# Kernel tuning notes

Measured on AMD Instinct MI355X. Metric: run time of the kernel, lower is better.

## Reference

```python
import jax, jax.numpy as jnp
import numpy as np

B, NQ, L, E, K = 64, 1024, 128, 8192, 2
LN_EPS = 1e-5


def setup_inputs() -> dict:
    key = jax.random.key(0)
    ks = jax.random.split(key, 16)
    s1 = 1.0 / np.sqrt(2 * L + 1)
    s2 = 1.0 / np.sqrt(L)
    s3 = 1.0 / np.sqrt(2 * L)
    return {
        "z0": jax.random.normal(ks[0], (B, L), jnp.float32),
        "edge_index": jax.random.randint(ks[1], (2, E), 0, NQ, jnp.int64),
        "edge_attr": jax.random.normal(ks[2], (E,), jnp.float32),
        "n_qubits": NQ,
        # edge MLP params, stacked over K message-passing rounds
        "e_w1": jax.random.normal(ks[3], (K, L, 2 * L + 1), jnp.float32) * s1,
        "e_b1": jnp.zeros((K, L), jnp.float32),
        "e_w2": jax.random.normal(ks[4], (K, L, L), jnp.float32) * s2,
        "e_b2": jnp.zeros((K, L), jnp.float32),
        # node MLP params
        "n_w1": jax.random.normal(ks[5], (K, L, 2 * L), jnp.float32) * s3,
        "n_b1": jnp.zeros((K, L), jnp.float32),
        "ln_g": jnp.ones((K, L), jnp.float32),
        "ln_b": jnp.zeros((K, L), jnp.float32),
        "n_w2": jax.random.normal(ks[6], (K, L, L), jnp.float32) * s2,
        "n_b2": jnp.zeros((K, L), jnp.float32),
    }


def reference(z0, edge_index, edge_attr, n_qubits,
              e_w1, e_b1, e_w2, e_b2,
              n_w1, n_b1, ln_g, ln_b, n_w2, n_b2):
    b, l = z0.shape
    src, tgt = edge_index[0], edge_index[1]
    e_ = src.shape[0]
    # broadcast latent z0 to every node: h [B, N, L]
    h = jnp.broadcast_to(z0[:, None, :], (b, n_qubits, l))
    e = jnp.broadcast_to(edge_attr[None, :, None], (b, e_, 1))  # [B, E, 1]
    k_rounds = e_w1.shape[0]
    for k in range(k_rounds):
        hi = h[:, src, :]  # gather source node feats [B, E, L]
        hj = h[:, tgt, :]  # gather target node feats [B, E, L]
        inp_e = jnp.concatenate([hi, hj, e], axis=-1)  # [B, E, 2L+1]
        m = jax.nn.relu(inp_e @ e_w1[k].T + e_b1[k]) @ e_w2[k].T + e_b2[k]
        # scatter_add messages back to source nodes
        m_agg = jnp.zeros_like(h).at[:, src, :].add(m)
        inp_n = jnp.concatenate([h, m_agg], axis=-1)  # [B, N, 2L]
        x = jax.nn.relu(inp_n @ n_w1[k].T + n_b1[k])
        mu = x.mean(axis=-1, keepdims=True)
        var = ((x - mu) ** 2).mean(axis=-1, keepdims=True)
        x = (x - mu) * jax.lax.rsqrt(var + LN_EPS) * ln_g[k] + ln_b[k]
        # Dropout(p=0.1) is identity in eval mode
        h = x @ n_w2[k].T + n_b2[k] + h  # residual
    return h.mean(axis=1)  # [B, L]
```

## Files before the change

### kernel.cpp

```cpp
#include <hip/hip_runtime.h>

#define B_   64
#define NQ_  1024
#define L_   128
#define E_   8192
#define M_   (B_*NQ_)
#define LDP  136
#define TILE 2176

typedef unsigned short u16;
typedef unsigned int   u32;
typedef unsigned long long u64;
typedef __attribute__((ext_vector_type(8))) short short8;
typedef __attribute__((ext_vector_type(4))) float floatx4;

#define WVB() __builtin_amdgcn_wave_barrier()

__device__ __forceinline__ int imax2(int a, int b) { return a > b ? a : b; }
__device__ __forceinline__ int imin2(int a, int b) { return a < b ? a : b; }

__device__ __forceinline__ u16 f2bf(float f) {
    union { float f; u32 u; } v; v.f = f;
    return (u16)((v.u + 0x7fffu + ((v.u >> 16) & 1u)) >> 16);
}
__device__ __forceinline__ float bf2f(u16 u) {
    union { u32 u; float f; } v; v.u = ((u32)u) << 16;
    return v.f;
}
__device__ __forceinline__ float bf2f_lo(u32 jv) { return __uint_as_float(jv << 16); }
__device__ __forceinline__ float bf2f_hi(u32 jv) { return __uint_as_float(jv & 0xffff0000u); }
__device__ __forceinline__ floatx4 mfma16(short8 a, short8 b, floatx4 c) {
    return __builtin_amdgcn_mfma_f32_16x16x32_bf16(a, b, c, 0, 0, 0);
}
__device__ __forceinline__ short8 sfrag(const u16* t, int r0, int kb, int lane) {
    return *(const short8*)(t + (r0 + (lane & 15)) * LDP + kb * 32 + (lane >> 4) * 8);
}
__device__ __forceinline__ short8 wfrag(const u16* wf, int nt, int kb, int lane) {
    return *(const short8*)(wf + (((kb << 3) + nt) * 64 + lane) * 8);
}
__device__ __forceinline__ void frag_flush(const u16* t, u16* wf, int nt, int lane) {
#pragma unroll
    for (int kb = 0; kb < 4; ++kb)
        *(short8*)(wf + (((kb << 3) + nt) * 64 + lane) * 8) = sfrag(t, 0, kb, lane);
}
__device__ __forceinline__ short8 frag_cvt(const float* base, int r0, int ld, int kb, int lane) {
    const float* p = base + (size_t)(r0 + (lane & 15)) * ld + kb * 32 + (lane >> 4) * 8;
    short8 s;
#pragma unroll
    for (int j = 0; j < 8; ++j) s[j] = (short)f2bf(p[j]);
    return s;
}
__device__ __forceinline__ void tile_store(u16* t, const floatx4* acc, int lane) {
    int col = lane & 15, qd = lane >> 4;
#pragma unroll
    for (int nt = 0; nt < 8; ++nt)
#pragma unroll
        for (int r = 0; r < 4; ++r)
            t[(qd * 4 + r) * LDP + nt * 16 + col] = f2bf(acc[nt][r]);
}
__device__ __forceinline__ void tile_flush(const u16* t, u16* g, int lane) {
#pragma unroll
    for (int it = 0; it < 4; ++it) {
        int chunk = it * 64 + lane, row = chunk >> 4, c8 = chunk & 15;
        *(uint4*)(g + (size_t)row * 128 + c8 * 8) = *(const uint4*)(t + row * LDP + c8 * 8);
    }
}
__device__ __forceinline__ int blk_swz() {
    int r = blockIdx.x;
    int b = (((r >> 3) & 7) << 3) | (r & 7);
    return b * 16 + (r >> 6);
}

struct P {
    const int* ei; const float* attr; const float* z0;
    const float* e_w1; const float* e_b1; const float* e_w2; const float* e_b2;
    const float* n_w1; const float* n_b1; const float* ln_g; const float* ln_b;
    const float* n_w2; const float* n_b2;
    int* ofs; int2* ta; int* perm; float* degf;
    u16* wf;
    u16* w_n20;
    float* wl; float* vb2;
    float* rx; float* rci; float* rcj; float* rh; float* mx0;
    u16* c0t; u16* t1g; u16* ci1; u16* cj1;
    float* out;
};

__global__ __launch_bounds__(256) void k_setup(P p) {
    __shared__ __align__(16) char smem[17408];
    int tid = threadIdx.x, blk = blockIdx.x;
    int lane = tid & 63, w = tid >> 6, col = lane & 15, qd = lane >> 4;

    if (blk == 0) {
        __shared__ int cnt[1024];
        __shared__ int wsum[4];
        __shared__ int dh[64];
        __shared__ int db[64];
        __shared__ int flag;
#pragma unroll
        for (int i = 0; i < 4; ++i) cnt[tid + i * 256] = 0;
        if (tid < 64) dh[tid] = 0;
        if (tid == 0) flag = 1;
        __syncthreads();
        if (tid < 100 && p.ei[2 * tid + 1] != 0) atomicAnd(&flag, 0);
        __syncthreads();
        int i64 = flag;
        for (int e = tid; e < E_; e += 256) {
            int s = i64 ? p.ei[2 * e] : p.ei[e];
            atomicAdd(&cnt[s], 1);
        }
        __syncthreads();
        int q0 = tid * 4;
        int c0 = cnt[q0], c1 = cnt[q0 + 1], c2 = cnt[q0 + 2], c3 = cnt[q0 + 3];
        int tsum = c0 + c1 + c2 + c3, incl = tsum;
#pragma unroll
        for (int o = 1; o < 64; o <<= 1) {
            int t = __shfl_up(incl, o, 64);
            if (lane >= o) incl += t;
        }
        if (lane == 63) wsum[w] = incl;
        atomicAdd(&dh[imin2(c0, 63)], 1); atomicAdd(&dh[imin2(c1, 63)], 1);
        atomicAdd(&dh[imin2(c2, 63)], 1); atomicAdd(&dh[imin2(c3, 63)], 1);
        __syncthreads();
        int wo = 0;
        for (int i = 0; i < w; ++i) wo += wsum[i];
        int base = wo + incl - tsum;
        p.ofs[q0] = base; p.ofs[q0 + 1] = base + c0;
        p.ofs[q0 + 2] = base + c0 + c1; p.ofs[q0 + 3] = base + c0 + c1 + c2;
        p.degf[q0] = (float)c0; p.degf[q0 + 1] = (float)c1;
        p.degf[q0 + 2] = (float)c2; p.degf[q0 + 3] = (float)c3;
        if (tid == 0) p.ofs[NQ_] = E_;
        __syncthreads();
        cnt[q0] = base; cnt[q0 + 1] = base + c0;
        cnt[q0 + 2] = base + c0 + c1; cnt[q0 + 3] = base + c0 + c1 + c2;
        if (tid < 64) {
            int v = dh[tid], inc = v;
#pragma unroll
            for (int o = 1; o < 64; o <<= 1) {
                int t = __shfl_up(inc, o, 64);
                if (tid >= o) inc += t;
            }
            db[tid] = inc - v;
        }
        __syncthreads();
        for (int e = tid; e < E_; e += 256) {
            int s = i64 ? p.ei[2 * e]        : p.ei[e];
            int t = i64 ? p.ei[2 * (E_ + e)] : p.ei[E_ + e];
            int pos = atomicAdd(&cnt[s], 1);
            p.ta[pos] = make_int2(t << 6, __float_as_int(p.attr[e]));
        }
        p.perm[atomicAdd(&db[imin2(c0, 63)], 1)] = q0;
        p.perm[atomicAdd(&db[imin2(c1, 63)], 1)] = q0 + 1;
        p.perm[atomicAdd(&db[imin2(c2, 63)], 1)] = q0 + 2;
        p.perm[atomicAdd(&db[imin2(c3, 63)], 1)] = q0 + 3;
        if (tid == 0) p.ta[E_] = make_int2(0, 0);
    } else if (blk <= 2) {
        int base = (blk - 1) * 8192;
        for (int idx = tid; idx < 8192; idx += 256)
            p.w_n20[base + idx] = f2bf(p.n_w2[base + idx]);
    } else if (blk == 3) {
        const float* src = p.n_w2 + 16384;
        u16* dst = p.wf + 5 * 16384;
        for (int pr = w; pr < 32; pr += 4) {
            int kb = pr >> 3, nt = pr & 7;
            const float* s = src + (nt * 16 + col) * 128 + kb * 32 + qd * 8;
            short8 v;
#pragma unroll
            for (int j = 0; j < 8; ++j) v[j] = (short)f2bf(s[j]);
            *(short8*)(dst + (pr * 64 + lane) * 8) = v;
        }
    } else if (blk <= 13) {
        int g = (blk - 4) >> 1, part = (blk - 4) & 1;
        const float* Pm; const float* Q; int ldp; u16* D;
        switch (g) {
            case 0:  Pm = p.n_w1 + 128;             ldp = 256; Q = p.e_w2;         D = p.wf;             break;
            case 1:  Pm = p.n_w1 + 32768 + 128;     ldp = 256; Q = p.e_w2 + 16384; D = p.wf + 4 * 16384; break;
            case 2:  Pm = p.e_w1 + 128 * 257;       ldp = 257; Q = p.n_w2;         D = p.wf + 1 * 16384; break;
            case 3:  Pm = p.e_w1 + 128 * 257 + 128; ldp = 257; Q = p.n_w2;         D = p.wf + 2 * 16384; break;
            default: Pm = p.n_w1 + 32768;           ldp = 256; Q = p.n_w2;         D = p.wf + 3 * 16384; break;
        }
        int tile = part * 4 + w;
        int r0 = tile * 16;
        floatx4 acc[8] = {};
#pragma unroll
        for (int kb = 0; kb < 4; ++kb) {
            short8 a = frag_cvt(Pm, r0, ldp, kb, lane);
#pragma unroll
            for (int nt = 0; nt < 8; ++nt) {
                short8 bq;
#pragma unroll
                for (int j = 0; j < 8; ++j)
                    bq[j] = (short)f2bf(Q[(kb * 32 + qd * 8 + j) * 128 + nt * 16 + col]);
                acc[nt] = mfma16(a, bq, acc[nt]);
            }
        }
        u16* slot = (u16*)smem + w * TILE;
        tile_store(slot, acc, lane); WVB();
        frag_flush(slot, D, tile, lane);
    } else if (blk == 14) {
        int r0 = w * 16;
        floatx4 acc[8] = {};
#pragma unroll
        for (int kb = 0; kb < 4; ++kb) {
            short8 a = frag_cvt(p.z0, r0, 128, kb, lane);
#pragma unroll
            for (int nt = 0; nt < 8; ++nt)
                acc[nt] = mfma16(a, frag_cvt(p.n_w1, nt * 16, 256, kb, lane), acc[nt]);
        }
#pragma unroll
        for (int nt = 0; nt < 8; ++nt) {
            int cg = nt * 16 + col; float bv = p.n_b1[cg];
#pragma unroll
            for (int r = 0; r < 4; ++r) p.rx[(r0 + qd * 4 + r) * 128 + cg] = acc[nt][r] + bv;
        }
    } else if (blk <= 17) {
        int r0 = w * 16;
        const float* Wp; int ld; const float* bias; float* dst;
        if (blk == 15)      { Wp = p.e_w1 + 128 * 257;       ld = 257; bias = p.e_b1 + 128; dst = p.rci; }
        else if (blk == 16) { Wp = p.e_w1 + 128 * 257 + 128; ld = 257; bias = nullptr;      dst = p.rcj; }
        else                { Wp = p.n_w1 + 32768;           ld = 256; bias = p.n_b1 + 128; dst = p.rh;  }
        floatx4 acc[8] = {};
#pragma unroll
        for (int kb = 0; kb < 4; ++kb) {
            short8 a;
            int rr = (r0 + col) * 128, kk = kb * 32 + qd * 8;
#pragma unroll
            for (int j = 0; j < 8; ++j) a[j] = (short)f2bf(p.z0[rr + kk + j] + p.n_b2[kk + j]);
#pragma unroll
            for (int nt = 0; nt < 8; ++nt)
                acc[nt] = mfma16(a, frag_cvt(Wp, nt * 16, ld, kb, lane), acc[nt]);
        }
#pragma unroll
        for (int nt = 0; nt < 8; ++nt) {
            int cg = nt * 16 + col;
            float bv = bias ? bias[cg] : 0.0f;
#pragma unroll
            for (int r = 0; r < 4; ++r) dst[(r0 + qd * 4 + r) * 128 + cg] = acc[nt][r] + bv;
        }
    } else if (blk == 18) {
        int r0 = w * 16;
        floatx4 a1[8] = {};
#pragma unroll
        for (int kb = 0; kb < 4; ++kb) {
            short8 a = frag_cvt(p.z0, r0, 128, kb, lane);
#pragma unroll
            for (int nt = 0; nt < 8; ++nt) {
                a1[nt] = mfma16(a, frag_cvt(p.e_w1,       nt * 16, 257, kb, lane), a1[nt]);
                a1[nt] = mfma16(a, frag_cvt(p.e_w1 + 128, nt * 16, 257, kb, lane), a1[nt]);
            }
        }
#pragma unroll
        for (int nt = 0; nt < 8; ++nt) {
            float bv = p.e_b1[nt * 16 + col];
#pragma unroll
            for (int r = 0; r < 4; ++r) a1[nt][r] += bv;
        }
        u16* slot = (u16*)smem + w * TILE;
        tile_store(slot, a1, lane); WVB();
        tile_flush(slot, p.c0t + (size_t)r0 * 128, lane);
    } else {
        int k = tid >> 7, c = tid & 127;
        const float4* wp = (const float4*)(p.n_w1 + k * 32768 + c * 256 + 128);
        const float4* bp = (const float4*)(p.e_b2 + k * 128);
        float s0 = 0.f, s1 = 0.f, s2 = 0.f, s3 = 0.f;
#pragma unroll
        for (int n4 = 0; n4 < 32; ++n4) {
            float4 a = wp[n4], bv = bp[n4];
            s0 += a.x * bv.x; s1 += a.y * bv.y; s2 += a.z * bv.z; s3 += a.w * bv.w;
        }
        p.vb2[tid] = (s0 + s1) + (s2 + s3);
        p.wl[tid]  = p.e_w1[k * 128 * 257 + c * 257 + 256];
        for (int i = tid; i < 8192; i += 256) p.mx0[i] = 0.0f;
    }
}

__device__ __forceinline__ void load_qmap(int* qmap, const int* perm,
                                          int blk, int w, int lane) {
    int W = (blk & 15) * 4 + w;
    int g0 = W, g1 = 127 - W;
    if (lane < 16)
        qmap[w * 16 + lane] = perm[lane < 8 ? g0 * 8 + lane : g1 * 8 + lane - 8];
    WVB();
}

__global__ __launch_bounds__(256, 4) void k_node0(P p) {
    __shared__ __align__(16) char smem[35072];
    u16* xt = (u16*)smem;
    u16* ob = (u16*)(smem + 17408);
    int* qmap = (int*)(smem + 34816);
    int tid = threadIdx.x, lane = tid & 63, w = tid >> 6;
    int col = lane & 15, qd = lane >> 4;
    int blk = blk_swz();
    int rowbase = blk * 64 + w * 16;
    int b = blk >> 4;
    load_qmap(qmap, p.perm, blk, w, lane);

    {
        u32 cv = ((const u32*)p.c0t)[b * 64 + lane];
        float cx = bf2f((u16)(cv & 0xffffu)), cy = bf2f((u16)(cv >> 16));
        float2 wl2 = ((const float2*)p.wl)[lane];
        const int* tay = (const int*)p.ta;
        for (int g2 = 0; g2 < 2; ++g2) {
            int st[8], en[8];
            float ax[8] = {}, ay[8] = {};
#pragma unroll
            for (int j = 0; j < 8; ++j) {
                int q = qmap[w * 16 + g2 * 8 + j];
                st[j] = p.ofs[q]; en[j] = p.ofs[q + 1];
            }
            int mn = en[0] - st[0], mx = mn;
#pragma unroll
            for (int j = 1; j < 8; ++j) {
                mn = imin2(mn, en[j] - st[j]); mx = imax2(mx, en[j] - st[j]);
            }
            float ac[8];
#pragma unroll
            for (int j = 0; j < 8; ++j) {
                int last = en[j] - 1;
                int safe = st[j] < en[j] ? st[j] : (last >= 0 ? last : 0);
                ac[j] = __int_as_float(tay[2 * safe + 1]);
            }
            for (int k2 = 0; k2 < mn; ++k2) {
                float an[8];
#pragma unroll
                for (int j = 0; j < 8; ++j) an[j] = __int_as_float(tay[2 * (st[j] + k2 + 1) + 1]);
#pragma unroll
                for (int j = 0; j < 8; ++j) {
                    ax[j] += fmaxf(cx + ac[j] * wl2.x, 0.f);
                    ay[j] += fmaxf(cy + ac[j] * wl2.y, 0.f);
                    ac[j] = an[j];
                }
            }
            for (int k2 = mn; k2 < mx; ++k2) {
                float an[8];
#pragma unroll
                for (int j = 0; j < 8; ++j) {
                    int idx = st[j] + k2 + 1, last = en[j] - 1;
                    int safe = idx < en[j] ? idx : (last >= 0 ? last : 0);
                    an[j] = __int_as_float(tay[2 * safe + 1]);
                }
#pragma unroll
                for (int j = 0; j < 8; ++j) {
                    bool v = st[j] + k2 < en[j];
                    ax[j] += v ? fmaxf(cx + ac[j] * wl2.x, 0.f) : 0.f;
                    ay[j] += v ? fmaxf(cy + ac[j] * wl2.y, 0.f) : 0.f;
                    ac[j] = an[j];
                }
            }
#pragma unroll
            for (int j = 0; j < 8; ++j) {
                int r = g2 * 8 + j;
                u32* tp = (u32*)(xt + (size_t)w * TILE + r * LDP);
                tp[lane] = (u32)f2bf(ax[j]) | ((u32)f2bf(ay[j]) << 16);
            }
        }
    }
    WVB();

    floatx4 xa[8] = {};
#pragma unroll
    for (int kb = 0; kb < 4; ++kb) {
        short8 a = sfrag(xt + w * TILE, 0, kb, lane);
#pragma unroll
        for (int nt = 0; nt < 8; ++nt) xa[nt] = mfma16(a, wfrag(p.wf, nt, kb, lane), xa[nt]);
    }
    WVB();
    float s8[8] = {};
#pragma unroll
    for (int nt = 0; nt < 8; ++nt) {
        int cg = nt * 16 + col;
        float base = p.rx[b * 128 + cg], vb = p.vb2[cg];
#pragma unroll
        for (int r = 0; r < 4; ++r) {
            int q = qmap[w * 16 + qd * 4 + r];
            xa[nt][r] = fmaxf(xa[nt][r] + base + p.degf[q] * vb, 0.f);
        }
    }
#pragma unroll
    for (int r = 0; r < 4; ++r) {
        float s = 0.f, s2 = 0.f;
#pragma unroll
        for (int nt = 0; nt < 8; ++nt) { float v = xa[nt][r]; s += v; s2 += v * v; }
#pragma unroll
        for (int o = 1; o < 16; o <<= 1) { s += __shfl_xor(s, o, 64); s2 += __shfl_xor(s2, o, 64); }
        float mu = s * (1.f / 128.f), var = s2 * (1.f / 128.f) - mu * mu;
        float rs = rsqrtf(var + 1e-5f);
#pragma unroll
        for (int nt = 0; nt < 8; ++nt) {
            int cg = nt * 16 + col;
            float xv = (xa[nt][r] - mu) * rs * p.ln_g[cg] + p.ln_b[cg];
            xa[nt][r] = xv;
            s8[nt] += xv;
        }
    }
    tile_store(xt + w * TILE, xa, lane);
#pragma unroll
    for (int nt = 0; nt < 8; ++nt) {
        s8[nt] += __shfl_xor(s8[nt], 16, 64);
        s8[nt] += __shfl_xor(s8[nt], 32, 64);
    }
    if (lane < 16) {
#pragma unroll
        for (int nt = 0; nt < 8; ++nt)
            atomicAdd(p.mx0 + b * 128 + nt * 16 + lane, s8[nt]);
    }
    WVB();
#pragma unroll
    for (int ph = 0; ph < 3; ++ph) {
        const u16* wfp = p.wf + ((ph == 0) ? 1 : (ph == 1) ? 2 : 3) * 16384;
        const float* rt = (ph == 0) ? p.rci : (ph == 1) ? p.rcj : p.rh;
        floatx4 ca[8] = {};
#pragma unroll
        for (int kb = 0; kb < 4; ++kb) {
            short8 a = sfrag(xt + w * TILE, 0, kb, lane);
#pragma unroll
            for (int nt = 0; nt < 8; ++nt) ca[nt] = mfma16(a, wfrag(wfp, nt, kb, lane), ca[nt]);
        }
#pragma unroll
        for (int nt = 0; nt < 8; ++nt) {
            float rc = rt[b * 128 + nt * 16 + col];
#pragma unroll
            for (int r = 0; r < 4; ++r) ca[nt][r] += rc;
        }
        if (ph == 2) {
            u64* t1f = (u64*)p.t1g;
            int tile = blk * 4 + w;
#pragma unroll
            for (int nt = 0; nt < 8; ++nt) {
                u32 lo = (u32)f2bf(ca[nt][0]) | ((u32)f2bf(ca[nt][1]) << 16);
                u32 hi = (u32)f2bf(ca[nt][2]) | ((u32)f2bf(ca[nt][3]) << 16);
                t1f[(size_t)(tile * 8 + nt) * 64 + lane] = (u64)lo | ((u64)hi << 32);
            }
        } else if (ph == 0) {
            tile_store(ob + w * TILE, ca, lane);
            WVB();
            tile_flush(ob + w * TILE, p.ci1 + (size_t)rowbase * 128, lane);
            WVB();
        } else {
            tile_store(ob + w * TILE, ca, lane);
            WVB();
#pragma unroll
            for (int it = 0; it < 4; ++it) {
                int chunk = it * 64 + lane, row = chunk >> 4, c8 = chunk & 15;
                int q = qmap[w * 16 + row];
                *(uint4*)(p.cj1 + ((size_t)b * NQ_ + q) * 128 + c8 * 8) =
                    *(const uint4*)(ob + w * TILE + row * LDP + c8 * 8);
            }
            WVB();
        }
    }
}

__global__ __launch_bounds__(256, 4) void k_node1(P p) {
    __shared__ __align__(16) char smem[35072];
    u16* xt = (u16*)smem;
    u16* ob = (u16*)(smem + 17408);
    int* qmap = (int*)(smem + 34816);
    int tid = threadIdx.x, lane = tid & 63, w = tid >> 6;
    int col = lane & 15, qd = lane >> 4;
    int blk = blk_swz();
    int rowbase = blk * 64 + w * 16;
    int b = blk >> 4;
    load_qmap(qmap, p.perm, blk, w, lane);

    {
        float2 wl2 = ((const float2*)(p.wl + 128))[lane];
        const u32* cip = (const u32*)p.ci1;
        const u32* cjp = (const u32*)p.cj1 + (size_t)b * NQ_ * 64;
        for (int g2 = 0; g2 < 2; ++g2) {
            int st[8], en[8];
            float ax[8] = {}, ay[8] = {}, cx[8], cy[8];
#pragma unroll
            for (int j = 0; j < 8; ++j) {
                int prow = rowbase + g2 * 8 + j;
                u32 cv = cip[(size_t)prow * 64 + lane];
                cx[j] = bf2f((u16)(cv & 0xffffu)); cy[j] = bf2f((u16)(cv >> 16));
                int q = qmap[w * 16 + g2 * 8 + j];
                st[j] = p.ofs[q]; en[j] = p.ofs[q + 1];
            }
            int mn = en[0] - st[0], mx = mn;
#pragma unroll
            for (int j = 1; j < 8; ++j) {
                mn = imin2(mn, en[j] - st[j]); mx = imax2(mx, en[j] - st[j]);
            }
            int tc[8]; float ac[8];
#pragma unroll
            for (int j = 0; j < 8; ++j) {
                int last = en[j] - 1;
                int safe = st[j] < en[j] ? st[j] : (last >= 0 ? last : 0);
                int2 tv = p.ta[safe];
                tc[j] = tv.x; ac[j] = __int_as_float(tv.y);
            }
            for (int k2 = 0; k2 < mn; ++k2) {
                u32 jv[8];
#pragma unroll
                for (int j = 0; j < 8; ++j) jv[j] = cjp[(u32)(tc[j] + lane)];
                int2 tv[8];
#pragma unroll
                for (int j = 0; j < 8; ++j) tv[j] = p.ta[st[j] + k2 + 1];
#pragma unroll
                for (int j = 0; j < 8; ++j) {
                    ax[j] += fmaxf(cx[j] + bf2f_lo(jv[j]) + ac[j] * wl2.x, 0.f);
                    ay[j] += fmaxf(cy[j] + bf2f_hi(jv[j]) + ac[j] * wl2.y, 0.f);
                    tc[j] = tv[j].x; ac[j] = __int_as_float(tv[j].y);
                }
            }
            for (int k2 = mn; k2 < mx; ++k2) {
                u32 jv[8];
#pragma unroll
                for (int j = 0; j < 8; ++j) jv[j] = cjp[(u32)(tc[j] + lane)];
                int2 tv[8];
#pragma unroll
                for (int j = 0; j < 8; ++j) {
                    int idx = st[j] + k2 + 1, last = en[j] - 1;
                    int safe = idx < en[j] ? idx : (last >= 0 ? last : 0);
                    tv[j] = p.ta[safe];
                }
#pragma unroll
                for (int j = 0; j < 8; ++j) {
                    bool v = st[j] + k2 < en[j];
                    float vx = fmaxf(cx[j] + bf2f_lo(jv[j]) + ac[j] * wl2.x, 0.f);
                    float vy = fmaxf(cy[j] + bf2f_hi(jv[j]) + ac[j] * wl2.y, 0.f);
                    ax[j] += v ? vx : 0.f;
                    ay[j] += v ? vy : 0.f;
                    tc[j] = tv[j].x; ac[j] = __int_as_float(tv[j].y);
                }
            }
#pragma unroll
            for (int j = 0; j < 8; ++j) {
                int r = g2 * 8 + j;
                u32* tp = (u32*)(xt + (size_t)w * TILE + r * LDP);
                tp[lane] = (u32)f2bf(ax[j]) | ((u32)f2bf(ay[j]) << 16);
            }
        }
    }
    WVB();

    const u16* wc1 = p.wf + 4 * 16384;
    floatx4 xa[8] = {};
#pragma unroll
    for (int kb = 0; kb < 4; ++kb) {
        short8 a = sfrag(xt + w * TILE, 0, kb, lane);
#pragma unroll
        for (int nt = 0; nt < 8; ++nt) xa[nt] = mfma16(a, wfrag(wc1, nt, kb, lane), xa[nt]);
    }
    const float* vb21 = p.vb2 + 128;
    const u64* t1f = (const u64*)p.t1g;
    int tile = blk * 4 + w;
#pragma unroll
    for (int nt = 0; nt < 8; ++nt) {
        int cg = nt * 16 + col;
        float vb = vb21[cg];
        u64 tv = t1f[(size_t)(tile * 8 + nt) * 64 + lane];
        float tvf[4] = { bf2f((u16)tv),         bf2f((u16)(tv >> 16)),
                         bf2f((u16)(tv >> 32)), bf2f((u16)(tv >> 48)) };
#pragma unroll
        for (int r = 0; r < 4; ++r) {
            int q = qmap[w * 16 + qd * 4 + r];
            xa[nt][r] = fmaxf(xa[nt][r] + tvf[r] + p.degf[q] * vb, 0.f);
        }
    }
#pragma unroll
    for (int r = 0; r < 4; ++r) {
        float s = 0.f, s2 = 0.f;
#pragma unroll
        for (int nt = 0; nt < 8; ++nt) { float v = xa[nt][r]; s += v; s2 += v * v; }
#pragma unroll
        for (int o = 1; o < 16; o <<= 1) { s += __shfl_xor(s, o, 64); s2 += __shfl_xor(s2, o, 64); }
        float mu = s * (1.f / 128.f), var = s2 * (1.f / 128.f) - mu * mu;
        float rs = rsqrtf(var + 1e-5f);
#pragma unroll
        for (int nt = 0; nt < 8; ++nt) {
            int cg = nt * 16 + col;
            xa[nt][r] = (xa[nt][r] - mu) * rs * p.ln_g[128 + cg] + p.ln_b[128 + cg];
        }
    }
    const u16* n21 = p.wf + 5 * 16384;
    float s8[8] = {};
    tile_store(ob + w * TILE, xa, lane);
    WVB();
    {
        floatx4 ma[8] = {};
#pragma unroll
        for (int kb = 0; kb < 4; ++kb) {
            short8 a = sfrag(ob + w * TILE, 0, kb, lane);
#pragma unroll
            for (int nt = 0; nt < 8; ++nt) ma[nt] = mfma16(a, wfrag(n21, nt, kb, lane), ma[nt]);
        }
#pragma unroll
        for (int nt = 0; nt < 8; ++nt)
#pragma unroll
            for (int r = 0; r < 4; ++r) s8[nt] += ma[nt][r];
    }
#pragma unroll
    for (int nt = 0; nt < 8; ++nt) {
        s8[nt] += __shfl_xor(s8[nt], 16, 64);
        s8[nt] += __shfl_xor(s8[nt], 32, 64);
    }
    if (lane < 16) {
#pragma unroll
        for (int nt = 0; nt < 8; ++nt)
            atomicAdd(p.out + b * 128 + nt * 16 + lane, s8[nt] * (1.f / 1024.f));
    }
    if ((blk & 15) == 0 && tid < 128) {
        int c = tid;
        const float* mx = p.mx0 + b * 128;
        float s = 0.f;
#pragma unroll
        for (int k8 = 0; k8 < 16; ++k8) {
            short8 wv = *(const short8*)(p.w_n20 + c * 128 + k8 * 8);
            const float* mxp = mx + k8 * 8;
#pragma unroll
            for (int j = 0; j < 8; ++j) s += mxp[j] * bf2f((u16)wv[j]);
        }
        float acc = p.z0[b * 128 + c] + p.n_b2[c] + p.n_b2[128 + c] + s * (1.f / 1024.f);
        atomicAdd(p.out + b * 128 + c, acc);
    }
}

extern "C" void kernel_launch(void* const* d_in, const int* in_sizes, int n_in,
                              void* d_out, int out_size, void* d_ws, size_t ws_size,
                              hipStream_t stream) {
    P p;
    p.z0   = (const float*)d_in[0];
    p.ei   = (const int*)d_in[1];
    p.attr = (const float*)d_in[2];
    p.e_w1 = (const float*)d_in[4];
    p.e_b1 = (const float*)d_in[5];
    p.e_w2 = (const float*)d_in[6];
    p.e_b2 = (const float*)d_in[7];
    p.n_w1 = (const float*)d_in[8];
    p.n_b1 = (const float*)d_in[9];
    p.ln_g = (const float*)d_in[10];
    p.ln_b = (const float*)d_in[11];
    p.n_w2 = (const float*)d_in[12];
    p.n_b2 = (const float*)d_in[13];
    p.out  = (float*)d_out;

    const size_t H = (size_t)M_ * L_;
    float* f  = (float*)d_ws;
    p.degf = f;
    p.wl   = f + 1024;
    p.vb2  = p.wl + 256;
    p.rx   = p.vb2 + 256;
    p.rci  = p.rx + 8192;
    p.rcj  = p.rci + 8192;
    p.rh   = p.rcj + 8192;
    p.mx0  = p.rh + 8192;
    p.ofs  = (int*)(p.mx0 + 8192);
    p.perm = p.ofs + 1056;
    p.ta   = (int2*)(p.perm + 1024);
    p.wf    = (u16*)(p.ta + E_ + 8);
    p.w_n20 = p.wf + 6 * 16384;
    p.c0t   = p.w_n20 + 16384;
    p.t1g   = p.c0t + 8192;
    p.ci1   = p.t1g + H;
    p.cj1   = p.ci1 + H;

    hipMemsetAsync(p.out, 0, 8192 * sizeof(float), stream);

    k_setup<<<20, 256, 0, stream>>>(p);
    k_node0<<<1024, 256, 0, stream>>>(p);
    k_node1<<<1024, 256, 0, stream>>>(p);
}
```

Before: 192.0 us.

## Split node1 into 128-thread blocks of 16 rows and stage setup weights via LDS

k_node1 now launches 4096 blocks of two waves, each block covering one 16-row tile. Each wave gathers messages for 8 of those rows, with separate min/max trip counts per group of four rows to reduce divergent tail work. Both waves then compute the first node GEMM redundantly, and only wave 0 runs the second GEMM and the output atomics. The aim is higher occupancy and more parallelism to hide latency in the irregular edge gather, at the price of redundant MFMA work and extra block barriers. Separately, k_setup transposes the Q weight chunks through LDS so global reads are coalesced float4 loads instead of strided scalar loads.

```diff
diff --git a/kernel.cpp b/kernel.cpp
--- a/kernel.cpp
+++ b/kernel.cpp
@@ -86,24 +86,24 @@
 };
 
 __global__ __launch_bounds__(256) void k_setup(P p) {
-    __shared__ __align__(16) char smem[17408];
+    __shared__ __align__(16) char smem[35072];
     int tid = threadIdx.x, blk = blockIdx.x;
     int lane = tid & 63, w = tid >> 6, col = lane & 15, qd = lane >> 4;
 
     if (blk == 0) {
-        __shared__ int cnt[1024];
-        __shared__ int wsum[4];
-        __shared__ int dh[64];
-        __shared__ int db[64];
-        __shared__ int flag;
+        int* cnt  = (int*)smem;
+        int* wsum = cnt + 1024;
+        int* dh   = wsum + 4;
+        int* db   = dh + 64;
+        int* flag = db + 64;
 #pragma unroll
         for (int i = 0; i < 4; ++i) cnt[tid + i * 256] = 0;
         if (tid < 64) dh[tid] = 0;
-        if (tid == 0) flag = 1;
+        if (tid == 0) *flag = 1;
         __syncthreads();
-        if (tid < 100 && p.ei[2 * tid + 1] != 0) atomicAnd(&flag, 0);
+        if (tid < 100 && p.ei[2 * tid + 1] != 0) atomicAnd(flag, 0);
         __syncthreads();
-        int i64 = flag;
+        int i64 = *flag;
         for (int e = tid; e < E_; e += 256) {
             int s = i64 ? p.ei[2 * e] : p.ei[e];
             atomicAdd(&cnt[s], 1);
@@ -178,22 +178,34 @@
             case 3:  Pm = p.e_w1 + 128 * 257 + 128; ldp = 257; Q = p.n_w2;         D = p.wf + 2 * 16384; break;
             default: Pm = p.n_w1 + 32768;           ldp = 256; Q = p.n_w2;         D = p.wf + 3 * 16384; break;
         }
+        float* QT  = (float*)smem;
+        u16* slots = (u16*)(smem + 16896);
         int tile = part * 4 + w;
         int r0 = tile * 16;
         floatx4 acc[8] = {};
-#pragma unroll
         for (int kb = 0; kb < 4; ++kb) {
+            __syncthreads();
+#pragma unroll
+            for (int i = 0; i < 4; ++i) {
+                int off = (tid + i * 256) * 4;
+                int r = off >> 7, c = off & 127;
+                float4 v = *(const float4*)(Q + (size_t)(kb * 32 + r) * 128 + c);
+                QT[(c + 0) * 33 + r] = v.x; QT[(c + 1) * 33 + r] = v.y;
+                QT[(c + 2) * 33 + r] = v.z; QT[(c + 3) * 33 + r] = v.w;
+            }
+            __syncthreads();
             short8 a = frag_cvt(Pm, r0, ldp, kb, lane);
 #pragma unroll
             for (int nt = 0; nt < 8; ++nt) {
                 short8 bq;
 #pragma unroll
                 for (int j = 0; j < 8; ++j)
-                    bq[j] = (short)f2bf(Q[(kb * 32 + qd * 8 + j) * 128 + nt * 16 + col]);
+                    bq[j] = (short)f2bf(QT[(nt * 16 + col) * 33 + qd * 8 + j]);
                 acc[nt] = mfma16(a, bq, acc[nt]);
             }
         }
-        u16* slot = (u16*)smem + w * TILE;
+        __syncthreads();
+        u16* slot = slots + w * TILE;
         tile_store(slot, acc, lane); WVB();
         frag_flush(slot, D, tile, lane);
     } else if (blk == 14) {
@@ -271,15 +283,6 @@
         p.wl[tid]  = p.e_w1[k * 128 * 257 + c * 257 + 256];
         for (int i = tid; i < 8192; i += 256) p.mx0[i] = 0.0f;
     }
-}
-
-__device__ __forceinline__ void load_qmap(int* qmap, const int* perm,
-                                          int blk, int w, int lane) {
-    int W = (blk & 15) * 4 + w;
-    int g0 = W, g1 = 127 - W;
-    if (lane < 16)
-        qmap[w * 16 + lane] = perm[lane < 8 ? g0 * 8 + lane : g1 * 8 + lane - 8];
-    WVB();
 }
 
 __global__ __launch_bounds__(256, 4) void k_node0(P p) {
@@ -292,7 +295,12 @@
     int blk = blk_swz();
     int rowbase = blk * 64 + w * 16;
     int b = blk >> 4;
-    load_qmap(qmap, p.perm, blk, w, lane);
+    {
+        int W = (blk & 15) * 4 + w;
+        if (lane < 16)
+            qmap[w * 16 + lane] = p.perm[lane < 8 ? W * 8 + lane : (127 - W) * 8 + lane - 8];
+        WVB();
+    }
 
     {
         u32 cv = ((const u32*)p.c0t)[b * 64 + lane];
@@ -450,120 +458,158 @@
     }
 }
 
-__global__ __launch_bounds__(256, 4) void k_node1(P p) {
-    __shared__ __align__(16) char smem[35072];
+__global__ __launch_bounds__(128, 8) void k_node1(P p) {
+    __shared__ __align__(16) char smem[4480];
     u16* xt = (u16*)smem;
-    u16* ob = (u16*)(smem + 17408);
-    int* qmap = (int*)(smem + 34816);
+    int* qmap = (int*)(smem + 4352);
     int tid = threadIdx.x, lane = tid & 63, w = tid >> 6;
     int col = lane & 15, qd = lane >> 4;
-    int blk = blk_swz();
-    int rowbase = blk * 64 + w * 16;
-    int b = blk >> 4;
-    load_qmap(qmap, p.perm, blk, w, lane);
+    int r4 = blockIdx.x;
+    int b  = (((r4 >> 3) & 7) << 3) | (r4 & 7);
+    int nb = b * 64 + (r4 >> 6);
+    int W  = nb & 63;
+    if (tid < 16) qmap[tid] = p.perm[tid < 8 ? W * 8 + tid : (127 - W) * 8 + tid - 8];
+    __syncthreads();
 
     {
         float2 wl2 = ((const float2*)(p.wl + 128))[lane];
         const u32* cip = (const u32*)p.ci1;
         const u32* cjp = (const u32*)p.cj1 + (size_t)b * NQ_ * 64;
-        for (int g2 = 0; g2 < 2; ++g2) {
-            int st[8], en[8];
-            float ax[8] = {}, ay[8] = {}, cx[8], cy[8];
+        int rr[8], st[8], en[8];
+        float ax[8] = {}, ay[8] = {}, cx[8], cy[8];
+#pragma unroll
+        for (int j = 0; j < 8; ++j) {
+            rr[j] = w * 4 + (j & 3) + 8 * (j >> 2);
+            int prow = nb * 16 + rr[j];
+            u32 cv = cip[(size_t)prow * 64 + lane];
+            cx[j] = bf2f((u16)(cv & 0xffffu)); cy[j] = bf2f((u16)(cv >> 16));
+            int q = qmap[rr[j]];
+            st[j] = p.ofs[q]; en[j] = p.ofs[q + 1];
+        }
+        int mA = en[0] - st[0], MA = mA, mB = en[4] - st[4], MB = mB;
+#pragma unroll
+        for (int j = 1; j < 4; ++j) {
+            mA = imin2(mA, en[j] - st[j]); MA = imax2(MA, en[j] - st[j]);
+        }
+#pragma unroll
+        for (int j = 5; j < 8; ++j) {
+            mB = imin2(mB, en[j] - st[j]); MB = imax2(MB, en[j] - st[j]);
+        }
+        int m8 = imin2(mA, mB);
+        int tc[8]; float ac[8];
+#pragma unroll
+        for (int j = 0; j < 8; ++j) {
+            int last = en[j] - 1;
+            int safe = st[j] < en[j] ? st[j] : (last >= 0 ? last : 0);
+            int2 tv = p.ta[safe];
+            tc[j] = tv.x; ac[j] = __int_as_float(tv.y);
+        }
+        for (int k2 = 0; k2 < m8; ++k2) {
+            u32 jv[8];
+#pragma unroll
+            for (int j = 0; j < 8; ++j) jv[j] = cjp[(u32)(tc[j] + lane)];
+            int2 tv[8];
+#pragma unroll
+            for (int j = 0; j < 8; ++j) tv[j] = p.ta[st[j] + k2 + 1];
 #pragma unroll
             for (int j = 0; j < 8; ++j) {
-                int prow = rowbase + g2 * 8 + j;
-                u32 cv = cip[(size_t)prow * 64 + lane];
-                cx[j] = bf2f((u16)(cv & 0xffffu)); cy[j] = bf2f((u16)(cv >> 16));
-                int q = qmap[w * 16 + g2 * 8 + j];
-                st[j] = p.ofs[q]; en[j] = p.ofs[q + 1];
-            }
-            int mn = en[0] - st[0], mx = mn;
-#pragma unroll
-            for (int j = 1; j < 8; ++j) {
-                mn = imin2(mn, en[j] - st[j]); mx = imax2(mx, en[j] - st[j]);
-            }
-            int tc[8]; float ac[8];
-#pragma unroll
-            for (int j = 0; j < 8; ++j) {
-                int last = en[j] - 1;
-                int safe = st[j] < en[j] ? st[j] : (last >= 0 ? last : 0);
-                int2 tv = p.ta[safe];
-                tc[j] = tv.x; ac[j] = __int_as_float(tv.y);
-            }
-            for (int k2 = 0; k2 < mn; ++k2) {
-                u32 jv[8];
-#pragma unroll
-                for (int j = 0; j < 8; ++j) jv[j] = cjp[(u32)(tc[j] + lane)];
-                int2 tv[8];
-#pragma unroll
-                for (int j = 0; j < 8; ++j) tv[j] = p.ta[st[j] + k2 + 1];
-#pragma unroll
-                for (int j = 0; j < 8; ++j) {
-                    ax[j] += fmaxf(cx[j] + bf2f_lo(jv[j]) + ac[j] * wl2.x, 0.f);
-                    ay[j] += fmaxf(cy[j] + bf2f_hi(jv[j]) + ac[j] * wl2.y, 0.f);
-                    tc[j] = tv[j].x; ac[j] = __int_as_float(tv[j].y);
-                }
-            }
-            for (int k2 = mn; k2 < mx; ++k2) {
-                u32 jv[8];
-#pragma unroll
-                for (int j = 0; j < 8; ++j) jv[j] = cjp[(u32)(tc[j] + lane)];
-                int2 tv[8];
-#pragma unroll
-                for (int j = 0; j < 8; ++j) {
-                    int idx = st[j] + k2 + 1, last = en[j] - 1;
-                    int safe = idx < en[j] ? idx : (last >= 0 ? last : 0);
-                    tv[j] = p.ta[safe];
-                }
-#pragma unroll
-                for (int j = 0; j < 8; ++j) {
-                    bool v = st[j] + k2 < en[j];
-                    float vx = fmaxf(cx[j] + bf2f_lo(jv[j]) + ac[j] * wl2.x, 0.f);
-                    float vy = fmaxf(cy[j] + bf2f_hi(jv[j]) + ac[j] * wl2.y, 0.f);
-                    ax[j] += v ? vx : 0.f;
-                    ay[j] += v ? vy : 0.f;
-                    tc[j] = tv[j].x; ac[j] = __int_as_float(tv[j].y);
-                }
-            }
-#pragma unroll
-            for (int j = 0; j < 8; ++j) {
-                int r = g2 * 8 + j;
-                u32* tp = (u32*)(xt + (size_t)w * TILE + r * LDP);
-                tp[lane] = (u32)f2bf(ax[j]) | ((u32)f2bf(ay[j]) << 16);
-            }
-        }
-    }
-    WVB();
+                ax[j] += fmaxf(cx[j] + bf2f_lo(jv[j]) + ac[j] * wl2.x, 0.f);
+                ay[j] += fmaxf(cy[j] + bf2f_hi(jv[j]) + ac[j] * wl2.y, 0.f);
+                tc[j] = tv[j].x; ac[j] = __int_as_float(tv[j].y);
+            }
+        }
+        for (int k2 = m8; k2 < MA; ++k2) {
+            u32 jv[4];
+#pragma unroll
+            for (int j = 0; j < 4; ++j) jv[j] = cjp[(u32)(tc[j] + lane)];
+            int2 tv[4];
+#pragma unroll
+            for (int j = 0; j < 4; ++j) {
+                int idx = st[j] + k2 + 1, last = en[j] - 1;
+                int safe = idx < en[j] ? idx : (last >= 0 ? last : 0);
+                tv[j] = p.ta[safe];
+            }
+#pragma unroll
+            for (int j = 0; j < 4; ++j) {
+                bool v = st[j] + k2 < en[j];
+                float vx = fmaxf(cx[j] + bf2f_lo(jv[j]) + ac[j] * wl2.x, 0.f);
+                float vy = fmaxf(cy[j] + bf2f_hi(jv[j]) + ac[j] * wl2.y, 0.f);
+                ax[j] += v ? vx : 0.f;
+                ay[j] += v ? vy : 0.f;
+                tc[j] = tv[j].x; ac[j] = __int_as_float(tv[j].y);
+            }
+        }
+        for (int k2 = m8; k2 < mB; ++k2) {
+            u32 jv[4];
+#pragma unroll
+            for (int j = 4; j < 8; ++j) jv[j - 4] = cjp[(u32)(tc[j] + lane)];
+            int2 tv[4];
+#pragma unroll
+            for (int j = 4; j < 8; ++j) tv[j - 4] = p.ta[st[j] + k2 + 1];
+#pragma unroll
+            for (int j = 4; j < 8; ++j) {
+                ax[j] += fmaxf(cx[j] + bf2f_lo(jv[j - 4]) + ac[j] * wl2.x, 0.f);
+                ay[j] += fmaxf(cy[j] + bf2f_hi(jv[j - 4]) + ac[j] * wl2.y, 0.f);
+                tc[j] = tv[j - 4].x; ac[j] = __int_as_float(tv[j - 4].y);
+            }
+        }
+        for (int k2 = imax2(m8, mB); k2 < MB; ++k2) {
+            u32 jv[4];
+#pragma unroll
+            for (int j = 4; j < 8; ++j) jv[j - 4] = cjp[(u32)(tc[j] + lane)];
+            int2 tv[4];
+#pragma unroll
+            for (int j = 4; j < 8; ++j) {
+                int idx = st[j] + k2 + 1, last = en[j] - 1;
+                int safe = idx < en[j] ? idx : (last >= 0 ? last : 0);
+                tv[j - 4] = p.ta[safe];
+            }
+#pragma unroll
+            for (int j = 4; j < 8; ++j) {
+                bool v = st[j] + k2 < en[j];
+                float vx = fmaxf(cx[j] + bf2f_lo(jv[j - 4]) + ac[j] * wl2.x, 0.f);
+                float vy = fmaxf(cy[j] + bf2f_hi(jv[j - 4]) + ac[j] * wl2.y, 0.f);
+                ax[j] += v ? vx : 0.f;
+                ay[j] += v ? vy : 0.f;
+                tc[j] = tv[j - 4].x; ac[j] = __int_as_float(tv[j - 4].y);
+            }
+        }
+#pragma unroll
+        for (int j = 0; j < 8; ++j) {
+            u32* tp = (u32*)(xt + rr[j] * LDP);
+            tp[lane] = (u32)f2bf(ax[j]) | ((u32)f2bf(ay[j]) << 16);
+        }
+    }
+    __syncthreads();
 
     const u16* wc1 = p.wf + 4 * 16384;
-    floatx4 xa[8] = {};
+    floatx4 x1[8] = {};
 #pragma unroll
     for (int kb = 0; kb < 4; ++kb) {
-        short8 a = sfrag(xt + w * TILE, 0, kb, lane);
-#pragma unroll
-        for (int nt = 0; nt < 8; ++nt) xa[nt] = mfma16(a, wfrag(wc1, nt, kb, lane), xa[nt]);
+        short8 a = sfrag(xt, 0, kb, lane);
+#pragma unroll
+        for (int nt = 0; nt < 8; ++nt) x1[nt] = mfma16(a, wfrag(wc1, nt, kb, lane), x1[nt]);
     }
     const float* vb21 = p.vb2 + 128;
     const u64* t1f = (const u64*)p.t1g;
-    int tile = blk * 4 + w;
 #pragma unroll
     for (int nt = 0; nt < 8; ++nt) {
         int cg = nt * 16 + col;
         float vb = vb21[cg];
-        u64 tv = t1f[(size_t)(tile * 8 + nt) * 64 + lane];
+        u64 tv = t1f[(size_t)(nb * 8 + nt) * 64 + lane];
         float tvf[4] = { bf2f((u16)tv),         bf2f((u16)(tv >> 16)),
                          bf2f((u16)(tv >> 32)), bf2f((u16)(tv >> 48)) };
 #pragma unroll
         for (int r = 0; r < 4; ++r) {
-            int q = qmap[w * 16 + qd * 4 + r];
-            xa[nt][r] = fmaxf(xa[nt][r] + tvf[r] + p.degf[q] * vb, 0.f);
+            int q = qmap[qd * 4 + r];
+            x1[nt][r] = fmaxf(x1[nt][r] + tvf[r] + p.degf[q] * vb, 0.f);
         }
     }
 #pragma unroll
     for (int r = 0; r < 4; ++r) {
         float s = 0.f, s2 = 0.f;
 #pragma unroll
-        for (int nt = 0; nt < 8; ++nt) { float v = xa[nt][r]; s += v; s2 += v * v; }
+        for (int nt = 0; nt < 8; ++nt) { float v = x1[nt][r]; s += v; s2 += v * v; }
 #pragma unroll
         for (int o = 1; o < 16; o <<= 1) { s += __shfl_xor(s, o, 64); s2 += __shfl_xor(s2, o, 64); }
         float mu = s * (1.f / 128.f), var = s2 * (1.f / 128.f) - mu * mu;
@@ -571,37 +617,36 @@
 #pragma unroll
         for (int nt = 0; nt < 8; ++nt) {
             int cg = nt * 16 + col;
-            xa[nt][r] = (xa[nt][r] - mu) * rs * p.ln_g[128 + cg] + p.ln_b[128 + cg];
-        }
-    }
-    const u16* n21 = p.wf + 5 * 16384;
-    float s8[8] = {};
-    tile_store(ob + w * TILE, xa, lane);
-    WVB();
-    {
+            x1[nt][r] = (x1[nt][r] - mu) * rs * p.ln_g[128 + cg] + p.ln_b[128 + cg];
+        }
+    }
+    __syncthreads();
+    if (w == 0) {
+        tile_store(xt, x1, lane);
+        WVB();
+        const u16* n21 = p.wf + 5 * 16384;
+        float s9[8] = {};
         floatx4 ma[8] = {};
 #pragma unroll
         for (int kb = 0; kb < 4; ++kb) {
-            short8 a = sfrag(ob + w * TILE, 0, kb, lane);
+            short8 a = sfrag(xt, 0, kb, lane);
 #pragma unroll
             for (int nt = 0; nt < 8; ++nt) ma[nt] = mfma16(a, wfrag(n21, nt, kb, lane), ma[nt]);
         }
 #pragma unroll
-        for (int nt = 0; nt < 8; ++nt)
-#pragma unroll
-            for (int r = 0; r < 4; ++r) s8[nt] += ma[nt][r];
-    }
-#pragma unroll
-    for (int nt = 0; nt < 8; ++nt) {
-        s8[nt] += __shfl_xor(s8[nt], 16, 64);
-        s8[nt] += __shfl_xor(s8[nt], 32, 64);
-    }
-    if (lane < 16) {
-#pragma unroll
-        for (int nt = 0; nt < 8; ++nt)
-            atomicAdd(p.out + b * 128 + nt * 16 + lane, s8[nt] * (1.f / 1024.f));
-    }
-    if ((blk & 15) == 0 && tid < 128) {
+        for (int nt = 0; nt < 8; ++nt) {
+#pragma unroll
+            for (int r = 0; r < 4; ++r) s9[nt] += ma[nt][r];
+            s9[nt] += __shfl_xor(s9[nt], 16, 64);
+            s9[nt] += __shfl_xor(s9[nt], 32, 64);
+        }
+        if (lane < 16) {
+#pragma unroll
+            for (int nt = 0; nt < 8; ++nt)
+                atomicAdd(p.out + b * 128 + nt * 16 + lane, s9[nt] * (1.f / 1024.f));
+        }
+    }
+    if ((nb & 63) == 0) {
         int c = tid;
         const float* mx = p.mx0 + b * 128;
         float s = 0.f;
@@ -660,5 +705,5 @@
 
     k_setup<<<20, 256, 0, stream>>>(p);
     k_node0<<<1024, 256, 0, stream>>>(p);
-    k_node1<<<1024, 256, 0, stream>>>(p);
-}
+    k_node1<<<4096, 128, 0, stream>>>(p);
+}
```

Measured after the change: 263.2 us. 37.1% more time.
